# Performance work log

Hardware: AMD Instinct MI355X
Metric: run time of the kernel (lower is better)

The kernel has to match this reference:

```python
import jax, jax.numpy as jnp
import numpy as np

B, E, D, NH, NP = 4, 32, 1024, 16, 4
LQ = E * E
DH = D // NH


def layer_norm(x, g, b, eps=1e-6):
    m = x.mean(-1, keepdims=True)
    v = ((x - m) ** 2).mean(-1, keepdims=True)
    return (x - m) / jnp.sqrt(v + eps) * g + b


def get_ref(H, W):
    # matches MSCrossAttnBlock.get_reference_points: centers normalized to [0,1], (x, y) order
    ys, xs = jnp.meshgrid((jnp.arange(H, dtype=jnp.float32) + 0.5) / H,
                          (jnp.arange(W, dtype=jnp.float32) + 0.5) / W, indexing='ij')
    return jnp.stack([xs.ravel(), ys.ravel()], -1)  # (H*W, 2)


def bilinear_sample(value_l, loc, H, W):
    # value_l: (N, nH, H*W, dh); loc: (N, Lq, nH, P, 2) normalized to [0,1]
    # replicates F.grid_sample(align_corners=False, padding_mode='zeros') with grid = 2*loc - 1
    N, Lq, nH, P, _ = loc.shape
    x = loc[..., 0] * W - 0.5
    y = loc[..., 1] * H - 0.5
    x0 = jnp.floor(x)
    y0 = jnp.floor(y)
    wx1 = x - x0
    wy1 = y - y0
    out = 0.0
    for dy, wy in ((0, 1.0 - wy1), (1, wy1)):
        for dx, wx in ((0, 1.0 - wx1), (1, wx1)):
            xi = x0 + dx
            yi = y0 + dy
            valid = (xi >= 0) & (xi < W) & (yi >= 0) & (yi < H)
            idx = (jnp.clip(yi, 0, H - 1) * W + jnp.clip(xi, 0, W - 1)).astype(jnp.int32)
            idx_t = idx.transpose(0, 2, 1, 3).reshape(N, nH, Lq * P)  # (N, nH, Lq*P)
            g = jnp.take_along_axis(value_l, idx_t[..., None], axis=2)  # (N, nH, Lq*P, dh)
            g = g.reshape(N, nH, Lq, P, -1).transpose(0, 2, 1, 3, 4)  # (N, Lq, nH, P, dh)
            w = (wx * wy) * valid.astype(value_l.dtype)
            out = out + g * w[..., None]
    return out


def msdeform(query, ref, inp, shapes, Wv, bv, Wo, bo, Wa, ba, Wp, bp):
    # MSDeformAttn forward (no padding mask)
    N, Lq, d = query.shape
    nL = len(shapes)
    value = (inp @ Wv.T + bv).reshape(N, -1, NH, DH).transpose(0, 2, 1, 3)  # (N, nH, Lin, dh)
    off = (query @ Wo.T + bo).reshape(N, Lq, NH, nL, NP, 2)
    attw = jax.nn.softmax((query @ Wa.T + ba).reshape(N, Lq, NH, nL * NP), axis=-1)
    attw = attw.reshape(N, Lq, NH, nL, NP)
    normalizer = jnp.array([[w, h] for (h, w) in shapes], dtype=query.dtype)  # (nL, 2) = [W, H]
    loc = ref[None, :, None, None, None, :] + off / normalizer[None, None, None, :, None, :]
    out = 0.0
    start = 0
    for l, (H, W) in enumerate(shapes):
        sampled = bilinear_sample(value[:, :, start:start + H * W], loc[:, :, :, l], H, W)
        out = out + (sampled * attw[:, :, :, l, :, None]).sum(3)  # (N, Lq, nH, dh)
        start += H * W
    return out.reshape(N, Lq, d) @ Wp.T + bp


def setup_inputs() -> dict:
    key = jax.random.key(0)
    ks = iter(jax.random.split(key, 64))
    def rnd(shape, scale):
        return jax.random.normal(next(ks), shape, dtype=jnp.float32) * scale
    inp = {}
    for i in range(4):
        inp[f'src{i}'] = rnd((B, LQ, D), 1.0)
    for nm in ('qn', 'fn', 'n1'):
        inp[nm + '_g'] = jnp.ones((D,), jnp.float32)
        inp[nm + '_b'] = jnp.zeros((D,), jnp.float32)
    inp['gamma1'] = rnd((D,), 0.1)
    inp['gamma2'] = rnd((D,), 0.1)
    ws = D ** -0.5
    for pre, nl in (('ca', 4), ('sa', 1)):
        inp[pre + '_vw'] = rnd((D, D), ws)
        inp[pre + '_vb'] = jnp.zeros((D,), jnp.float32)
        inp[pre + '_ow'] = rnd((NH * nl * NP * 2, D), ws)
        inp[pre + '_ob'] = rnd((NH * nl * NP * 2,), 0.1)
        inp[pre + '_aw'] = rnd((NH * nl * NP, D), ws)
        inp[pre + '_ab'] = jnp.zeros((NH * nl * NP,), jnp.float32)
        inp[pre + '_pw'] = rnd((D, D), ws)
        inp[pre + '_pb'] = jnp.zeros((D,), jnp.float32)
    return inp


def reference(src0, src1, src2, src3, qn_g, qn_b, fn_g, fn_b, n1_g, n1_b, gamma1, gamma2,
              ca_vw, ca_vb, ca_ow, ca_ob, ca_aw, ca_ab, ca_pw, ca_pb,
              sa_vw, sa_vb, sa_ow, sa_ob, sa_aw, sa_ab, sa_pw, sa_pb):
    shapes4 = [(E, E)] * 4
    feat = jnp.concatenate([src0, src1, src2, src3], axis=1)  # (B, 4*LQ, D)
    query = src3  # srcs[-1], pos embed is None
    ref = get_ref(E, E)  # (LQ, 2)
    attn = msdeform(layer_norm(query, qn_g, qn_b), ref, layer_norm(feat, fn_g, fn_b),
                    shapes4, ca_vw, ca_vb, ca_ow, ca_ob, ca_aw, ca_ab, ca_pw, ca_pb)
    attn1 = layer_norm(attn, n1_g, n1_b)
    attn2 = msdeform(attn1, ref, attn1, [(E, E)],
                     sa_vw, sa_vb, sa_ow, sa_ob, sa_aw, sa_ab, sa_pw, sa_pb)
    attn = attn + gamma2 * attn2
    return query + gamma1 * attn
```

## Files before the change

kernel.cpp:

```cpp
#include <hip/hip_runtime.h>


#define DEV __device__ __forceinline__

typedef float f32x4 __attribute__((ext_vector_type(4)));
typedef __bf16 bf16x8 __attribute__((ext_vector_type(8)));

DEV unsigned short f2bf(float f) {
  union { float f; unsigned u; } a; a.f = f;
  unsigned r = a.u + 0x7fffu + ((a.u >> 16) & 1u);
  return (unsigned short)(r >> 16);
}
DEV float bf2f(unsigned short h) {
  union { unsigned u; float f; } a; a.u = ((unsigned)h) << 16;
  return a.f;
}

DEV void gl_lds16(const unsigned short* g, unsigned short* l) {
  __builtin_amdgcn_global_load_lds(
      (const __attribute__((address_space(1))) void*)g,
      (__attribute__((address_space(3))) void*)l, 16, 0, 0);
}

struct CvtArgs {
  const float* src[8];
  unsigned short* dst;
  int off4[9];
};

__global__ __launch_bounds__(256) void f2bf_multi(CvtArgs a) {
  int i = blockIdx.x * 256 + threadIdx.x;
  int seg = 0;
  #pragma unroll
  for (int s = 1; s < 8; ++s) seg += (i >= a.off4[s]) ? 1 : 0;
  const float4 v = ((const float4*)a.src[seg])[i - a.off4[seg]];
  unsigned short* o = a.dst + (size_t)i * 4;
  o[0] = f2bf(v.x); o[1] = f2bf(v.y); o[2] = f2bf(v.z); o[3] = f2bf(v.w);
}

DEV void ln_row_wave(const float* __restrict__ xr, const float* __restrict__ g,
                     const float* __restrict__ b,
                     unsigned short* __restrict__ op_row) {
  const int lane = threadIdx.x & 63;
  float4 v[4];
  float s = 0.f, s2 = 0.f;
  #pragma unroll
  for (int j = 0; j < 4; ++j) {
    v[j] = ((const float4*)xr)[lane + 64 * j];
    s  += v[j].x + v[j].y + v[j].z + v[j].w;
    s2 += v[j].x*v[j].x + v[j].y*v[j].y + v[j].z*v[j].z + v[j].w*v[j].w;
  }
  #pragma unroll
  for (int o = 32; o; o >>= 1) { s += __shfl_xor(s, o); s2 += __shfl_xor(s2, o); }
  const float mean = s * (1.f / 1024.f);
  const float rstd = rsqrtf(s2 * (1.f / 1024.f) - mean * mean + 1e-6f);
  #pragma unroll
  for (int j = 0; j < 4; ++j) {
    float4 gg = ((const float4*)g)[lane + 64 * j];
    float4 bb = ((const float4*)b)[lane + 64 * j];
    ushort4 r;
    r.x = f2bf((v[j].x - mean) * rstd * gg.x + bb.x);
    r.y = f2bf((v[j].y - mean) * rstd * gg.y + bb.y);
    r.z = f2bf((v[j].z - mean) * rstd * gg.z + bb.z);
    r.w = f2bf((v[j].w - mean) * rstd * gg.w + bb.w);
    ((ushort4*)op_row)[lane + 64 * j] = r;
  }
}

__global__ __launch_bounds__(256) void ln_wave_kernel(
    const float* __restrict__ x, const float* __restrict__ g,
    const float* __restrict__ b, unsigned short* __restrict__ out) {
  int row = blockIdx.x * 4 + (threadIdx.x >> 6);
  ln_row_wave(x + (size_t)row * 1024, g, b, out + (size_t)row * 1024);
}

__global__ __launch_bounds__(256) void ln5_wave_kernel(
    const float* __restrict__ s0, const float* __restrict__ s1,
    const float* __restrict__ s2, const float* __restrict__ s3,
    const float* __restrict__ fg, const float* __restrict__ fb,
    const float* __restrict__ qg, const float* __restrict__ qb,
    unsigned short* __restrict__ f_out, unsigned short* __restrict__ q_out) {
  int row = blockIdx.x * 4 + (threadIdx.x >> 6);
  if (row < 16384) {
    int l = row >> 12, inner = row & 4095;
    const float* srcs[4] = {s0, s1, s2, s3};
    int orow = (inner >> 10) * 4096 + l * 1024 + (inner & 1023);
    ln_row_wave(srcs[l] + (size_t)inner * 1024, fg, fb,
                f_out + (size_t)orow * 1024);
  } else {
    int inner = row - 16384;
    ln_row_wave(s3 + (size_t)inner * 1024, qg, qb,
                q_out + (size_t)inner * 1024);
  }
}

struct GemmP {
  const unsigned short* A; const unsigned short* W;
  void* C; void* C1; void* C2;
  const float* b0; const float* b1; const float* b2;
  const float* src3; const float* g1; const float* g2; const float* attnp;
  int M, N, K, tilesM;
};

template <int BM, int BN, int EPI>
DEV void gemm_body(const GemmP& P, int id, unsigned short* smem) {
  constexpr int WMT = BM / 2, WNT = BN / 2;
  constexpr int MF = WMT / 16, NF = WNT / 16;
  constexpr int PA = BM / 64, PB = BN / 64;
  constexpr int BUF = (BM + BN) * 64;
  const int tid = threadIdx.x;
  const int wave = tid >> 6, lane = tid & 63;
  const int wm = (wave & 1) * WMT, wn = (wave >> 1) * WNT;
  const int m0 = (id % P.tilesM) * BM;
  const int n0 = (id / P.tilesM) * BN;
  const int lq = lane >> 4, lm = lane & 15;
  const int r16 = lane >> 2;
  const int cst = lane & 3;
  const int csrc = cst ^ ((r16 >> 1) & 3);
  const int aslot = lq ^ ((lm >> 1) & 3);

  f32x4 acc[MF][NF] = {};
  const int kTiles = P.K >> 6;

  const unsigned short* gA[PA];
  #pragma unroll
  for (int p = 0; p < PA; ++p) {
    int grow = m0 + (wave + 4 * p) * 16 + r16;
    gA[p] = P.A + (size_t)grow * P.K + csrc * 8;
  }
  const unsigned short* gB[PB];
  #pragma unroll
  for (int p = 0; p < PB; ++p) {
    int grow = min(n0 + (wave + 4 * p) * 16 + r16, P.N - 1);
    gB[p] = P.W + (size_t)grow * P.K + csrc * 8;
  }

  auto stage = [&](int b, int t) {
    unsigned short* bA = smem + b * BUF;
    unsigned short* bB = bA + BM * 64;
    const int k0 = t << 6;
    #pragma unroll
    for (int s = 0; s < 2; ++s) {
      #pragma unroll
      for (int p = 0; p < PA; ++p)
        gl_lds16(gA[p] + k0 + s * 32,
                 bA + s * BM * 32 + (wave + 4 * p) * 512);
      #pragma unroll
      for (int p = 0; p < PB; ++p)
        gl_lds16(gB[p] + k0 + s * 32,
                 bB + s * BN * 32 + (wave + 4 * p) * 512);
    }
  };

  stage(0, 0);
  __syncthreads();
  int cur = 0;
  #pragma unroll 1
  for (int t = 0; t < kTiles; ++t) {
    if (t + 1 < kTiles) stage(cur ^ 1, t + 1);
    const unsigned short* bA = smem + cur * BUF;
    const unsigned short* bB = bA + BM * 64;
    #pragma unroll
    for (int s = 0; s < 2; ++s) {
      bf16x8 af[MF], bfr[NF];
      #pragma unroll
      for (int mi = 0; mi < MF; ++mi)
        af[mi] = *(const bf16x8*)(bA + s * BM * 32 + ((wm >> 4) + mi) * 512 + lm * 32 + aslot * 8);
      #pragma unroll
      for (int ni = 0; ni < NF; ++ni)
        bfr[ni] = *(const bf16x8*)(bB + s * BN * 32 + ((wn >> 4) + ni) * 512 + lm * 32 + aslot * 8);
      #pragma unroll
      for (int mi = 0; mi < MF; ++mi)
        #pragma unroll
        for (int ni = 0; ni < NF; ++ni)
          acc[mi][ni] = __builtin_amdgcn_mfma_f32_16x16x32_bf16(
              af[mi], bfr[ni], acc[mi][ni], 0, 0, 0);
    }
    __syncthreads();
    cur ^= 1;
  }

  #pragma unroll
  for (int mi = 0; mi < MF; ++mi) {
    #pragma unroll
    for (int ni = 0; ni < NF; ++ni) {
      const int col = n0 + wn + ni * 16 + lm;
      #pragma unroll
      for (int r2 = 0; r2 < 4; ++r2) {
        const int row = m0 + wm + mi * 16 + lq * 4 + r2;
        float v = acc[mi][ni][r2];
        if constexpr (EPI == 0) {
          ((float*)P.C)[(size_t)row * 1024 + col] = v + P.b0[col];
        } else if constexpr (EPI == 1) {
          ((unsigned short*)P.C)[(size_t)row * 1024 + col] = f2bf(v + P.b0[col]);
        } else if constexpr (EPI == 2) {
          if (col < 512)
            ((float*)P.C)[(size_t)row * 512 + col] = v + P.b0[col];
          else
            ((float*)P.C1)[(size_t)row * 256 + col - 512] = v + P.b1[col - 512];
        } else if constexpr (EPI == 3) {
          if (col < 1024)
            ((unsigned short*)P.C)[(size_t)row * 1024 + col] = f2bf(v + P.b0[col]);
          else if (col < 1152)
            ((float*)P.C1)[(size_t)row * 128 + col - 1024] = v + P.b1[col - 1024];
          else if (col < 1216)
            ((float*)P.C2)[(size_t)row * 64 + col - 1152] = v + P.b2[col - 1152];
        } else {
          size_t i = (size_t)row * 1024 + col;
          float vv = v + P.b0[col];
          ((float*)P.C)[i] = P.src3[i] + P.g1[col] * (P.attnp[i] + P.g2[col] * vv);
        }
      }
    }
  }
}

template <int BM, int BN, int EPI>
__global__ __launch_bounds__(256) void gemm_v3(GemmP P) {
  extern __shared__ __align__(16) unsigned short smem[];
  gemm_body<BM, BN, EPI>(P, blockIdx.x, smem);
}

__global__ __launch_bounds__(512, 2) void gemm256(GemmP P) {
  __shared__ __align__(16) unsigned short smem[65536];
  const int tid = threadIdx.x;
  const int wave = tid >> 6, lane = tid & 63;
  const int wm = (wave & 1) * 128, wn = (wave >> 1) * 64;
  const int m0 = (blockIdx.x & 63) * 256;
  const int n0 = (blockIdx.x >> 6) * 256;
  const int lq = lane >> 4, lm = lane & 15;
  const int r16 = lane >> 2, cst = lane & 3;
  const int csrc = cst ^ ((r16 >> 1) & 3);
  const int aslot = lq ^ ((lm >> 1) & 3);
  const int K = P.K;
  const int kT = K >> 6;

  const int gA0 = (wave & 3) + ((wave >> 2) << 3);
  const int gB2 = ((wave >> 1) << 2) + (wave & 1);
  const unsigned short* baseA0 =
      P.A + (size_t)(m0 + gA0 * 16 + r16) * K + csrc * 8;
  const unsigned short* baseA1 = baseA0 + (size_t)64 * K;
  const unsigned short* baseB2 =
      P.W + (size_t)(n0 + gB2 * 16 + r16) * K + csrc * 8;
  const unsigned short* baseB3 = baseB2 + (size_t)32 * K;
  const int ldsA0 = gA0 * 512 + lane * 8;
  const int ldsA1 = (gA0 + 4) * 512 + lane * 8;
  const int ldsB2 = 16384 + gB2 * 512 + lane * 8;
  const int ldsB3 = 16384 + (gB2 + 2) * 512 + lane * 8;

  auto stg = [&](const unsigned short* gbase, int ldsOff, int buf, int tsrc) {
    const unsigned short* g = gbase + tsrc * 64;
    unsigned short* l = smem + buf * 32768 + ldsOff;
    gl_lds16(g, l);
    gl_lds16(g + 32, l + 8192);
  };

  const int aBase = (wave & 1) * 8;
  const int bBase = (wave >> 1) * 4;
  const int rdI = lm * 32 + aslot * 8;

  auto rdA = [&](int buf, int s, int gi) {
    return *(const bf16x8*)(smem + buf * 32768 + s * 8192 + (aBase + gi) * 512 + rdI);
  };
  auto rdB = [&](int buf, int s, int gi) {
    return *(const bf16x8*)(smem + buf * 32768 + 16384 + s * 8192 + (bBase + gi) * 512 + rdI);
  };

  f32x4 acc[8][4] = {};
  bf16x8 a[2][4], b0[2][2], b1[2][2];

#define VMB8() asm volatile("s_waitcnt vmcnt(8)\ns_barrier" ::: "memory")

  stg(baseA0, ldsA0, 0, 0);
  stg(baseB2, ldsB2, 0, 0);
  stg(baseB3, ldsB3, 0, 0);
  stg(baseA1, ldsA1, 0, 0);
  stg(baseA0, ldsA0, 1, min(1, kT - 1));
  stg(baseB2, ldsB2, 1, min(1, kT - 1));

  auto iterate = [&](int t, int c) {
    const int nc = c ^ 1;
    const int t1 = min(t + 1, kT - 1);
    const int t2 = min(t + 2, kT - 1);
    VMB8();
    stg(baseB3, ldsB3, nc, t1);
    #pragma unroll
    for (int s = 0; s < 2; ++s) {
      #pragma unroll
      for (int i = 0; i < 4; ++i) a[s][i] = rdA(c, s, i);
      #pragma unroll
      for (int i = 0; i < 2; ++i) b0[s][i] = rdB(c, s, i);
    }
    __builtin_amdgcn_s_setprio(1);
    #pragma unroll
    for (int s = 0; s < 2; ++s)
      #pragma unroll
      for (int mi = 0; mi < 4; ++mi)
        #pragma unroll
        for (int ni = 0; ni < 2; ++ni)
          acc[mi][ni] = __builtin_amdgcn_mfma_f32_16x16x32_bf16(
              a[s][mi], b0[s][ni], acc[mi][ni], 0, 0, 0);
    __builtin_amdgcn_s_setprio(0);
    VMB8();
    stg(baseA1, ldsA1, nc, t1);
    #pragma unroll
    for (int s = 0; s < 2; ++s)
      #pragma unroll
      for (int i = 0; i < 2; ++i) b1[s][i] = rdB(c, s, 2 + i);
    __builtin_amdgcn_s_setprio(1);
    #pragma unroll
    for (int s = 0; s < 2; ++s)
      #pragma unroll
      for (int mi = 0; mi < 4; ++mi)
        #pragma unroll
        for (int ni = 0; ni < 2; ++ni)
          acc[mi][2 + ni] = __builtin_amdgcn_mfma_f32_16x16x32_bf16(
              a[s][mi], b1[s][ni], acc[mi][2 + ni], 0, 0, 0);
    __builtin_amdgcn_s_setprio(0);
    VMB8();
    stg(baseA0, ldsA0, c, t2);
    #pragma unroll
    for (int s = 0; s < 2; ++s)
      #pragma unroll
      for (int i = 0; i < 4; ++i) a[s][i] = rdA(c, s, 4 + i);
    __builtin_amdgcn_s_setprio(1);
    #pragma unroll
    for (int s = 0; s < 2; ++s)
      #pragma unroll
      for (int mi = 0; mi < 4; ++mi)
        #pragma unroll
        for (int ni = 0; ni < 2; ++ni)
          acc[4 + mi][ni] = __builtin_amdgcn_mfma_f32_16x16x32_bf16(
              a[s][mi], b0[s][ni], acc[4 + mi][ni], 0, 0, 0);
    __builtin_amdgcn_s_setprio(0);
    VMB8();
    stg(baseB2, ldsB2, c, t2);
    __builtin_amdgcn_s_setprio(1);
    #pragma unroll
    for (int s = 0; s < 2; ++s)
      #pragma unroll
      for (int mi = 0; mi < 4; ++mi)
        #pragma unroll
        for (int ni = 0; ni < 2; ++ni)
          acc[4 + mi][2 + ni] = __builtin_amdgcn_mfma_f32_16x16x32_bf16(
              a[s][mi], b1[s][ni], acc[4 + mi][2 + ni], 0, 0, 0);
    __builtin_amdgcn_s_setprio(0);
  };

  #pragma unroll 1
  for (int t = 0; t < kT; t += 2) {
    iterate(t, 0);
    iterate(t + 1, 1);
  }
  asm volatile("s_waitcnt vmcnt(0)" ::: "memory");
#undef VMB8

  #pragma unroll
  for (int mi = 0; mi < 8; ++mi) {
    #pragma unroll
    for (int ni = 0; ni < 4; ++ni) {
      const int col = n0 + wn + ni * 16 + lm;
      #pragma unroll
      for (int r2 = 0; r2 < 4; ++r2) {
        const int row = m0 + wm + mi * 16 + lq * 4 + r2;
        ((unsigned short*)P.C)[(size_t)row * 1024 + col] =
            f2bf(acc[mi][ni][r2] + P.b0[col]);
      }
    }
  }
}

template <int NLEV>
__global__ __launch_bounds__(256) void ms_sample_fused(
    const unsigned short* __restrict__ value, const float* __restrict__ off,
    const float* __restrict__ logits, unsigned short* __restrict__ out) {
  const int nq = blockIdx.x;
  const int wave = threadIdx.x >> 6, lane = threadIdx.x & 63;
  const int h = (wave << 2) + (lane >> 4);
  const int c = (lane & 15) << 2;
  const int q = nq & 1023, n = nq >> 10;
  const float* offp = off + ((size_t)nq * 16 + h) * (NLEV * 8);
  const float* lgp  = logits + ((size_t)nq * 16 + h) * (NLEV * 4);

  float lg[NLEV * 4];
  #pragma unroll
  for (int i = 0; i < NLEV; ++i) {
    float4 v = ((const float4*)lgp)[i];
    lg[4*i] = v.x; lg[4*i+1] = v.y; lg[4*i+2] = v.z; lg[4*i+3] = v.w;
  }
  float mx = lg[0];
  #pragma unroll
  for (int i = 1; i < NLEV * 4; ++i) mx = fmaxf(mx, lg[i]);
  float ssum = 0.f;
  #pragma unroll
  for (int i = 0; i < NLEV * 4; ++i) { lg[i] = __expf(lg[i] - mx); ssum += lg[i]; }
  const float inv = 1.f / ssum;

  const float fqx = (float)(q & 31), fqy = (float)(q >> 5);
  float a0 = 0.f, a1 = 0.f, a2 = 0.f, a3 = 0.f;

  #pragma unroll
  for (int l = 0; l < NLEV; ++l) {
    const unsigned short* vl =
        value + ((size_t)(n * NLEV + l) << 20) + h * 64 + c;
    #pragma unroll
    for (int p = 0; p < 4; ++p) {
      float2 o2 = ((const float2*)offp)[l * 4 + p];
      float aw = lg[l * 4 + p] * inv;
      float xx = fqx + o2.x, yy = fqy + o2.y;
      float xf = floorf(xx), yf = floorf(yy);
      float fx = xx - xf, fy = yy - yf;
      int ix = (int)xf, iy = (int)yf;
      int ix1 = ix + 1, iy1 = iy + 1;
      float vx0 = ((unsigned)ix  < 32u) ? 1.f : 0.f;
      float vx1 = ((unsigned)ix1 < 32u) ? 1.f : 0.f;
      float vy0 = ((unsigned)iy  < 32u) ? 1.f : 0.f;
      float vy1 = ((unsigned)iy1 < 32u) ? 1.f : 0.f;
      int cx0 = min(max(ix, 0), 31), cx1 = min(max(ix1, 0), 31);
      int cy0 = min(max(iy, 0), 31), cy1 = min(max(iy1, 0), 31);
      float w00 = (1.f - fx) * (1.f - fy) * vx0 * vy0 * aw;
      float w01 = fx * (1.f - fy) * vx1 * vy0 * aw;
      float w10 = (1.f - fx) * fy * vx0 * vy1 * aw;
      float w11 = fx * fy * vx1 * vy1 * aw;
      ushort4 u00 = *(const ushort4*)(vl + ((size_t)(cy0 * 32 + cx0) << 10));
      ushort4 u01 = *(const ushort4*)(vl + ((size_t)(cy0 * 32 + cx1) << 10));
      ushort4 u10 = *(const ushort4*)(vl + ((size_t)(cy1 * 32 + cx0) << 10));
      ushort4 u11 = *(const ushort4*)(vl + ((size_t)(cy1 * 32 + cx1) << 10));
      a0 += w00 * bf2f(u00.x) + w01 * bf2f(u01.x) + w10 * bf2f(u10.x) + w11 * bf2f(u11.x);
      a1 += w00 * bf2f(u00.y) + w01 * bf2f(u01.y) + w10 * bf2f(u10.y) + w11 * bf2f(u11.y);
      a2 += w00 * bf2f(u00.z) + w01 * bf2f(u01.z) + w10 * bf2f(u10.z) + w11 * bf2f(u11.z);
      a3 += w00 * bf2f(u00.w) + w01 * bf2f(u01.w) + w10 * bf2f(u10.w) + w11 * bf2f(u11.w);
    }
  }
  ushort4 r;
  r.x = f2bf(a0); r.y = f2bf(a1); r.z = f2bf(a2); r.w = f2bf(a3);
  *(ushort4*)(out + ((size_t)nq * 16 + h) * 64 + c) = r;
}

extern "C" void kernel_launch(void* const* d_in, const int* in_sizes, int n_in,
                              void* d_out, int out_size, void* d_ws,
                              size_t ws_size, hipStream_t stream) {
  (void)in_sizes; (void)n_in; (void)out_size; (void)ws_size;
  const float* src[4] = {(const float*)d_in[0], (const float*)d_in[1],
                         (const float*)d_in[2], (const float*)d_in[3]};
  const float* qn_g = (const float*)d_in[4];
  const float* qn_b = (const float*)d_in[5];
  const float* fn_g = (const float*)d_in[6];
  const float* fn_b = (const float*)d_in[7];
  const float* n1_g = (const float*)d_in[8];
  const float* n1_b = (const float*)d_in[9];
  const float* gamma1 = (const float*)d_in[10];
  const float* gamma2 = (const float*)d_in[11];
  const float* ca_vw = (const float*)d_in[12];
  const float* ca_vb = (const float*)d_in[13];
  const float* ca_ow = (const float*)d_in[14];
  const float* ca_ob = (const float*)d_in[15];
  const float* ca_aw = (const float*)d_in[16];
  const float* ca_ab = (const float*)d_in[17];
  const float* ca_pw = (const float*)d_in[18];
  const float* ca_pb = (const float*)d_in[19];
  const float* sa_vw = (const float*)d_in[20];
  const float* sa_vb = (const float*)d_in[21];
  const float* sa_ow = (const float*)d_in[22];
  const float* sa_ob = (const float*)d_in[23];
  const float* sa_aw = (const float*)d_in[24];
  const float* sa_ab = (const float*)d_in[25];
  const float* sa_pw = (const float*)d_in[26];
  const float* sa_pb = (const float*)d_in[27];

  char* wsp = (char*)d_ws;
  size_t off = 0;
  auto alloc = [&](size_t bytes) {
    char* r = wsp + off;
    off = (off + bytes + 255) & ~(size_t)255;
    return r;
  };
  const size_t MB = 1024 * 1024;
  unsigned short* w_ca_vw = (unsigned short*)alloc(1024 * 1024 * 2);
  unsigned short* w_ca_ow = (unsigned short*)alloc(512 * 1024 * 2);
  unsigned short* w_ca_aw = (unsigned short*)alloc(256 * 1024 * 2);
  unsigned short* w_ca_pw = (unsigned short*)alloc(1024 * 1024 * 2);
  unsigned short* w_sa_vw = (unsigned short*)alloc(1024 * 1024 * 2);
  unsigned short* w_sa_ow = (unsigned short*)alloc(128 * 1024 * 2);
  unsigned short* w_sa_aw = (unsigned short*)alloc(64 * 1024 * 2);
  unsigned short* w_sa_pw = (unsigned short*)alloc(1024 * 1024 * 2);
  (void)w_ca_aw; (void)w_sa_ow; (void)w_sa_aw;
  char* R1 = alloc(32 * MB);
  char* R2 = alloc(32 * MB);
  char* R3 = alloc(8 * MB);
  char* R4 = alloc(8 * MB);
  char* R5 = alloc(4 * MB);

  unsigned short* f_ln    = (unsigned short*)R1;
  float*          attn    = (float*)R1;
  unsigned short* attn1   = (unsigned short*)(R1 + 16 * MB);
  unsigned short* samp_sa = (unsigned short*)(R1 + 24 * MB);
  unsigned short* val_ca  = (unsigned short*)R2;
  unsigned short* val_sa  = (unsigned short*)R2;
  unsigned short* q_ln    = (unsigned short*)R3;
  unsigned short* samp_ca = (unsigned short*)R3;
  float*          off_ca  = (float*)R4;
  float*          off_sa  = (float*)R4;
  float*          attw_sa = (float*)(R4 + 4 * MB);
  float*          attw_ca = (float*)R5;

  CvtArgs ca;
  ca.src[0] = ca_vw; ca.src[1] = ca_ow; ca.src[2] = ca_aw; ca.src[3] = ca_pw;
  ca.src[4] = sa_vw; ca.src[5] = sa_ow; ca.src[6] = sa_aw; ca.src[7] = sa_pw;
  ca.dst = w_ca_vw;
  const int sizes4[8] = {262144, 131072, 65536, 262144, 262144, 32768, 16384, 262144};
  ca.off4[0] = 0;
  for (int i = 0; i < 8; ++i) ca.off4[i + 1] = ca.off4[i] + sizes4[i];
  f2bf_multi<<<ca.off4[8] / 256, 256, 0, stream>>>(ca);

  ln5_wave_kernel<<<5120, 256, 0, stream>>>(src[0], src[1], src[2], src[3],
                                            fn_g, fn_b, qn_g, qn_b, f_ln, q_ln);

  auto mkP = [](const unsigned short* A, const unsigned short* W, void* C,
                const float* b0, int M, int N, int K, int tilesM) {
    GemmP p{}; p.A = A; p.W = W; p.C = C; p.b0 = b0;
    p.M = M; p.N = N; p.K = K; p.tilesM = tilesM;
    return p;
  };

  constexpr int LDS_128 = 2 * (128 + 128) * 64 * 2;
  constexpr int LDS_64  = 2 * (64 + 128) * 64 * 2;

  gemm256<<<256, 512, 0, stream>>>(
      mkP(f_ln, w_ca_vw, val_ca, ca_vb, 16384, 1024, 1024, 64));
  {
    GemmP po = mkP(q_ln, w_ca_ow, off_ca, ca_ob, 4096, 768, 1024, 32);
    po.C1 = attw_ca; po.b1 = ca_ab;
    gemm_v3<128, 128, 2><<<192, 256, LDS_128, stream>>>(po);
  }

  ms_sample_fused<4><<<4096, 256, 0, stream>>>(val_ca, off_ca, attw_ca, samp_ca);
  gemm_v3<64, 128, 0><<<64 * 8, 256, LDS_64, stream>>>(
      mkP(samp_ca, w_ca_pw, attn, ca_pb, 4096, 1024, 1024, 64));

  ln_wave_kernel<<<1024, 256, 0, stream>>>(attn, n1_g, n1_b, attn1);
  {
    GemmP p = mkP(attn1, w_sa_vw, val_sa, sa_vb, 4096, 1216, 1024, 64);
    p.C1 = off_sa; p.b1 = sa_ob; p.C2 = attw_sa; p.b2 = sa_ab;
    gemm_v3<64, 128, 3><<<64 * 10, 256, LDS_64, stream>>>(p);
  }
  ms_sample_fused<1><<<4096, 256, 0, stream>>>(val_sa, off_sa, attw_sa, samp_sa);
  {
    GemmP p = mkP(samp_sa, w_sa_pw, d_out, sa_pb, 4096, 1024, 1024, 64);
    p.src3 = src[3]; p.g1 = gamma1; p.g2 = gamma2; p.attnp = attn;
    gemm_v3<64, 128, 4><<<64 * 8, 256, LDS_64, stream>>>(p);
  }
}
```

Before: 355.3 us.

## Precompute sampling weights in LDS and enlarge projection GEMM tiles to 128x128

The sampling kernel now computes the softmax (via wave shuffles), bilinear weights and base offsets once per (head, point) into shared-memory tables. Previously each of the 16 lanes sharing a head recomputed them redundantly. The inner loop then only reads the tables and performs four gathers, at the cost of a __syncthreads and LDS usage. Separately, the three 4096-row GEMMs switch from 64x128 to 128x128 tiles, halving the block count to reduce A/B reload traffic, though fewer blocks may underfill the GPU.

```diff
diff --git a/kernel.cpp b/kernel.cpp
--- a/kernel.cpp
+++ b/kernel.cpp
@@ -374,63 +374,75 @@
 __global__ __launch_bounds__(256) void ms_sample_fused(
     const unsigned short* __restrict__ value, const float* __restrict__ off,
     const float* __restrict__ logits, unsigned short* __restrict__ out) {
+  constexpr int NPTS = NLEV * 4;
+  constexpr int STR = NPTS + 1;
+  __shared__ float4 wTab[16 * STR];
+  __shared__ int2  iTab[16 * STR];
   const int nq = blockIdx.x;
-  const int wave = threadIdx.x >> 6, lane = threadIdx.x & 63;
+  const int tid = threadIdx.x;
+  const int q = nq & 1023, n = nq >> 10;
+
+  if (tid < 16 * NPTS) {
+    const int h1 = tid / NPTS;
+    const int p1 = tid - h1 * NPTS;
+    float lg = logits[((size_t)nq * 16 + h1) * NPTS + p1];
+    float mx = lg;
+    #pragma unroll
+    for (int m = 1; m < NPTS; m <<= 1) mx = fmaxf(mx, __shfl_xor(mx, m));
+    const float e = __expf(lg - mx);
+    float sum = e;
+    #pragma unroll
+    for (int m = 1; m < NPTS; m <<= 1) sum += __shfl_xor(sum, m);
+    const float aw = e / sum;
+    const float2 o2 =
+        ((const float2*)(off + ((size_t)nq * 16 + h1) * NPTS * 2))[p1];
+    const float fqx = (float)(q & 31), fqy = (float)(q >> 5);
+    float xx = fqx + o2.x, yy = fqy + o2.y;
+    float xf = floorf(xx), yf = floorf(yy);
+    float fx = xx - xf, fy = yy - yf;
+    int ix = (int)xf, iy = (int)yf;
+    int ix1 = ix + 1, iy1 = iy + 1;
+    float vx0 = ((unsigned)ix  < 32u) ? 1.f : 0.f;
+    float vx1 = ((unsigned)ix1 < 32u) ? 1.f : 0.f;
+    float vy0 = ((unsigned)iy  < 32u) ? 1.f : 0.f;
+    float vy1 = ((unsigned)iy1 < 32u) ? 1.f : 0.f;
+    int cx0 = min(max(ix, 0), 31), cx1 = min(max(ix1, 0), 31);
+    int cy0 = min(max(iy, 0), 31), cy1 = min(max(iy1, 0), 31);
+    float4 w;
+    w.x = (1.f - fx) * (1.f - fy) * vx0 * vy0 * aw;
+    w.y = fx * (1.f - fy) * vx1 * vy0 * aw;
+    w.z = (1.f - fx) * fy * vx0 * vy1 * aw;
+    w.w = fx * fy * vx1 * vy1 * aw;
+    const int l = p1 >> 2;
+    int2 io;
+    io.x = ((n * NLEV + l) << 20) + ((cy0 * 32 + cx0) << 10);
+    io.y = (cx1 - cx0) | ((cy1 - cy0) << 1);
+    wTab[h1 * STR + p1] = w;
+    iTab[h1 * STR + p1] = io;
+  }
+  __syncthreads();
+
+  const int wave = tid >> 6, lane = tid & 63;
   const int h = (wave << 2) + (lane >> 4);
   const int c = (lane & 15) << 2;
-  const int q = nq & 1023, n = nq >> 10;
-  const float* offp = off + ((size_t)nq * 16 + h) * (NLEV * 8);
-  const float* lgp  = logits + ((size_t)nq * 16 + h) * (NLEV * 4);
-
-  float lg[NLEV * 4];
-  #pragma unroll
-  for (int i = 0; i < NLEV; ++i) {
-    float4 v = ((const float4*)lgp)[i];
-    lg[4*i] = v.x; lg[4*i+1] = v.y; lg[4*i+2] = v.z; lg[4*i+3] = v.w;
-  }
-  float mx = lg[0];
-  #pragma unroll
-  for (int i = 1; i < NLEV * 4; ++i) mx = fmaxf(mx, lg[i]);
-  float ssum = 0.f;
-  #pragma unroll
-  for (int i = 0; i < NLEV * 4; ++i) { lg[i] = __expf(lg[i] - mx); ssum += lg[i]; }
-  const float inv = 1.f / ssum;
-
-  const float fqx = (float)(q & 31), fqy = (float)(q >> 5);
+  const unsigned short* __restrict__ vb = value + h * 64 + c;
   float a0 = 0.f, a1 = 0.f, a2 = 0.f, a3 = 0.f;
 
-  #pragma unroll
-  for (int l = 0; l < NLEV; ++l) {
-    const unsigned short* vl =
-        value + ((size_t)(n * NLEV + l) << 20) + h * 64 + c;
-    #pragma unroll
-    for (int p = 0; p < 4; ++p) {
-      float2 o2 = ((const float2*)offp)[l * 4 + p];
-      float aw = lg[l * 4 + p] * inv;
-      float xx = fqx + o2.x, yy = fqy + o2.y;
-      float xf = floorf(xx), yf = floorf(yy);
-      float fx = xx - xf, fy = yy - yf;
-      int ix = (int)xf, iy = (int)yf;
-      int ix1 = ix + 1, iy1 = iy + 1;
-      float vx0 = ((unsigned)ix  < 32u) ? 1.f : 0.f;
-      float vx1 = ((unsigned)ix1 < 32u) ? 1.f : 0.f;
-      float vy0 = ((unsigned)iy  < 32u) ? 1.f : 0.f;
-      float vy1 = ((unsigned)iy1 < 32u) ? 1.f : 0.f;
-      int cx0 = min(max(ix, 0), 31), cx1 = min(max(ix1, 0), 31);
-      int cy0 = min(max(iy, 0), 31), cy1 = min(max(iy1, 0), 31);
-      float w00 = (1.f - fx) * (1.f - fy) * vx0 * vy0 * aw;
-      float w01 = fx * (1.f - fy) * vx1 * vy0 * aw;
-      float w10 = (1.f - fx) * fy * vx0 * vy1 * aw;
-      float w11 = fx * fy * vx1 * vy1 * aw;
-      ushort4 u00 = *(const ushort4*)(vl + ((size_t)(cy0 * 32 + cx0) << 10));
-      ushort4 u01 = *(const ushort4*)(vl + ((size_t)(cy0 * 32 + cx1) << 10));
-      ushort4 u10 = *(const ushort4*)(vl + ((size_t)(cy1 * 32 + cx0) << 10));
-      ushort4 u11 = *(const ushort4*)(vl + ((size_t)(cy1 * 32 + cx1) << 10));
-      a0 += w00 * bf2f(u00.x) + w01 * bf2f(u01.x) + w10 * bf2f(u10.x) + w11 * bf2f(u11.x);
-      a1 += w00 * bf2f(u00.y) + w01 * bf2f(u01.y) + w10 * bf2f(u10.y) + w11 * bf2f(u11.y);
-      a2 += w00 * bf2f(u00.z) + w01 * bf2f(u01.z) + w10 * bf2f(u10.z) + w11 * bf2f(u11.z);
-      a3 += w00 * bf2f(u00.w) + w01 * bf2f(u01.w) + w10 * bf2f(u10.w) + w11 * bf2f(u11.w);
-    }
+  #pragma unroll 4
+  for (int p = 0; p < NPTS; ++p) {
+    const float4 w = wTab[h * STR + p];
+    const int2 io = iTab[h * STR + p];
+    const unsigned short* b = vb + io.x;
+    const int sx = (io.y & 1) << 10;
+    const int sy = (io.y & 2) << 14;
+    ushort4 u00 = *(const ushort4*)(b);
+    ushort4 u01 = *(const ushort4*)(b + sx);
+    ushort4 u10 = *(const ushort4*)(b + sy);
+    ushort4 u11 = *(const ushort4*)(b + sx + sy);
+    a0 += w.x * bf2f(u00.x) + w.y * bf2f(u01.x) + w.z * bf2f(u10.x) + w.w * bf2f(u11.x);
+    a1 += w.x * bf2f(u00.y) + w.y * bf2f(u01.y) + w.z * bf2f(u10.y) + w.w * bf2f(u11.y);
+    a2 += w.x * bf2f(u00.z) + w.y * bf2f(u01.z) + w.z * bf2f(u10.z) + w.w * bf2f(u11.z);
+    a3 += w.x * bf2f(u00.w) + w.y * bf2f(u01.w) + w.z * bf2f(u10.w) + w.w * bf2f(u11.w);
   }
   ushort4 r;
   r.x = f2bf(a0); r.y = f2bf(a1); r.z = f2bf(a2); r.w = f2bf(a3);
@@ -524,7 +536,6 @@
   };
 
   constexpr int LDS_128 = 2 * (128 + 128) * 64 * 2;
-  constexpr int LDS_64  = 2 * (64 + 128) * 64 * 2;
 
   gemm256<<<256, 512, 0, stream>>>(
       mkP(f_ln, w_ca_vw, val_ca, ca_vb, 16384, 1024, 1024, 64));
@@ -535,19 +546,19 @@
   }
 
   ms_sample_fused<4><<<4096, 256, 0, stream>>>(val_ca, off_ca, attw_ca, samp_ca);
-  gemm_v3<64, 128, 0><<<64 * 8, 256, LDS_64, stream>>>(
-      mkP(samp_ca, w_ca_pw, attn, ca_pb, 4096, 1024, 1024, 64));
+  gemm_v3<128, 128, 0><<<256, 256, LDS_128, stream>>>(
+      mkP(samp_ca, w_ca_pw, attn, ca_pb, 4096, 1024, 1024, 32));
 
   ln_wave_kernel<<<1024, 256, 0, stream>>>(attn, n1_g, n1_b, attn1);
   {
-    GemmP p = mkP(attn1, w_sa_vw, val_sa, sa_vb, 4096, 1216, 1024, 64);
+    GemmP p = mkP(attn1, w_sa_vw, val_sa, sa_vb, 4096, 1216, 1024, 32);
     p.C1 = off_sa; p.b1 = sa_ob; p.C2 = attw_sa; p.b2 = sa_ab;
-    gemm_v3<64, 128, 3><<<64 * 10, 256, LDS_64, stream>>>(p);
+    gemm_v3<128, 128, 3><<<320, 256, LDS_128, stream>>>(p);
   }
   ms_sample_fused<1><<<4096, 256, 0, stream>>>(val_sa, off_sa, attw_sa, samp_sa);
   {
-    GemmP p = mkP(samp_sa, w_sa_pw, d_out, sa_pb, 4096, 1024, 1024, 64);
+    GemmP p = mkP(samp_sa, w_sa_pw, d_out, sa_pb, 4096, 1024, 1024, 32);
     p.src3 = src[3]; p.g1 = gamma1; p.g2 = gamma2; p.attnp = attn;
-    gemm_v3<64, 128, 4><<<64 * 8, 256, LDS_64, stream>>>(p);
-  }
-}
+    gemm_v3<128, 128, 4><<<256, 256, LDS_128, stream>>>(p);
+  }
+}
```

Measured after the change: 365.9 us. +3.0%, slower.
